# Optimization experiments

Measured on AMD Instinct MI355X. Metric: run time of the kernel, lower is better.

Reference implementation:

```python
import jax, jax.numpy as jnp
import numpy as np

B, L, D_IN, D_MODEL, H = 8, 1024, 256, 512, 8
D_HEAD = D_MODEL // H


def setup_inputs() -> dict:
    key = jax.random.key(0)
    ks = jax.random.split(key, 12)
    queries = jax.random.normal(ks[0], (B, L, D_IN), dtype=jnp.float32)
    keys_ = jax.random.normal(ks[1], (B, L, D_IN), dtype=jnp.float32)
    values = jax.random.normal(ks[2], (B, L, D_IN), dtype=jnp.float32)
    attention_mask = jnp.ones((B, L), dtype=jnp.int32)
    # binary symmetric-ish adjacency (sparse molecular graph style)
    adjacency_matrix = (jax.random.uniform(ks[3], (B, L, L)) < 0.05).astype(jnp.float32)
    distance_matrix = jax.random.uniform(ks[4], (B, L, L), dtype=jnp.float32) * 10.0
    s = 1.0 / np.sqrt(D_IN)
    W_q = jax.random.normal(ks[5], (D_MODEL, D_IN), dtype=jnp.float32) * s
    W_k = jax.random.normal(ks[6], (D_MODEL, D_IN), dtype=jnp.float32) * s
    W_v = jax.random.normal(ks[7], (D_MODEL, D_IN), dtype=jnp.float32) * s
    W_o = jax.random.normal(ks[8], (D_MODEL, D_MODEL), dtype=jnp.float32) / np.sqrt(D_MODEL)
    lambda_a = jax.random.normal(ks[9], (H,), dtype=jnp.float32) * 0.1
    lambda_d = jax.random.normal(ks[10], (H,), dtype=jnp.float32) * 0.1
    return {"queries": queries, "keys": keys_, "values": values,
            "attention_mask": attention_mask, "adjacency_matrix": adjacency_matrix,
            "distance_matrix": distance_matrix, "W_q": W_q, "W_k": W_k,
            "W_v": W_v, "W_o": W_o, "lambda_a": lambda_a, "lambda_d": lambda_d}


def _split_heads(x):
    # (b, l, d_model) -> (b, h, l, d_head)
    b, l, _ = x.shape
    return x.reshape(b, l, H, D_HEAD).transpose(0, 2, 1, 3)


def reference(queries, keys, values, attention_mask, adjacency_matrix,
              distance_matrix, W_q, W_k, W_v, W_o, lambda_a, lambda_d):
    Q = _split_heads(queries @ W_q.T)   # (b,h,l,d)
    K = _split_heads(keys @ W_k.T)
    V = _split_heads(values @ W_v.T)
    scores = jnp.einsum("bhqd,bhkd->bhqk", Q, K) / jnp.sqrt(jnp.asarray(D_HEAD, Q.dtype))
    # MSRSA: per-head learned scalars inject graph structure into the scores
    scores = (scores
              + lambda_a[None, :, None, None] * adjacency_matrix[:, None, :, :]
              + lambda_d[None, :, None, None] * distance_matrix[:, None, :, :])
    mask = attention_mask[:, None, None, :] > 0  # (b,1,1,l) key mask
    scores = jnp.where(mask, scores, jnp.asarray(-1e9, scores.dtype))
    attn_weight = jax.nn.softmax(scores, axis=-1)  # (b,h,l,l)
    out = jnp.einsum("bhqk,bhkd->bhqd", attn_weight, V)
    out = out.transpose(0, 2, 1, 3).reshape(queries.shape[0], queries.shape[1], D_MODEL)
    return out @ W_o.T
```

## Files before the change

### kernel.cpp

```cpp
#include <hip/hip_runtime.h>
#include <hip/hip_fp16.h>

#define BB 8
#define LL 1024
#define DIN 256
#define DM 512
#define HH 8
#define DH 64

typedef __attribute__((ext_vector_type(8))) short bf16x8;
typedef __attribute__((ext_vector_type(4))) float f32x4;

__device__ __forceinline__ unsigned short f2bf(float f) {
  union { float f; unsigned u; } c; c.f = f;
  unsigned u = c.u;
  return (unsigned short)((u + 0x7fffu + ((u >> 16) & 1u)) >> 16);
}

#if defined(__has_builtin)
#if __has_builtin(__builtin_amdgcn_cvt_pk_bf16_f32)
#define HAS_PK_BF16 1
#endif
#endif

#ifdef HAS_PK_BF16
typedef __bf16 bf2 __attribute__((ext_vector_type(2)));
__device__ __forceinline__ unsigned pk2(float lo, float hi) {
  union { bf2 v; unsigned u; } c;
  c.v = __builtin_amdgcn_cvt_pk_bf16_f32(lo, hi);
  return c.u;
}
#else
__device__ __forceinline__ unsigned pk2(float lo, float hi) {
  return ((unsigned)f2bf(hi) << 16) | f2bf(lo);
}
#endif

__device__ __forceinline__ unsigned pkh(float a, float d) {
  return (unsigned)__half_as_ushort(__float2half_rn(a)) |
         ((unsigned)__half_as_ushort(__float2half_rn(d)) << 16);
}

__device__ __forceinline__ void async_copy16(void* lds, const void* g) {
  __builtin_amdgcn_global_load_lds(
      (const __attribute__((address_space(1))) unsigned*)g,
      (__attribute__((address_space(3))) unsigned*)lds, 16, 0, 0);
}

__global__ __launch_bounds__(256) void prep(
    const float* __restrict__ qin, const float* __restrict__ kin,
    const float* __restrict__ vin,
    const float* __restrict__ wq, const float* __restrict__ wk,
    const float* __restrict__ wv, const float* __restrict__ wo,
    const int* __restrict__ msk,
    const float* __restrict__ adj, const float* __restrict__ dis,
    unsigned short* __restrict__ xq, unsigned short* __restrict__ xk,
    unsigned short* __restrict__ xv,
    unsigned short* __restrict__ wqb, unsigned short* __restrict__ wkb,
    unsigned short* __restrict__ wvb, unsigned short* __restrict__ wob,
    float* __restrict__ mad, unsigned* __restrict__ bp)
{
  int t = blockIdx.x * 256 + threadIdx.x;
  const int XS = 524288, WS = 32768;
  if (t < 3 * XS) {
    int seg = t >> 19, off = t & (XS - 1);
    const float* s = (seg == 0) ? qin : (seg == 1) ? kin : vin;
    unsigned short* d = (seg == 0) ? xq : (seg == 1) ? xk : xv;
    float4 f = ((const float4*)s)[off];
    uint2 o = { pk2(f.x, f.y), pk2(f.z, f.w) };
    ((uint2*)d)[off] = o;
    return;
  }
  t -= 3 * XS;
  if (t < 3 * WS) {
    int seg = t >> 15, off = t & (WS - 1);
    const float* s = (seg == 0) ? wq : (seg == 1) ? wk : wv;
    unsigned short* d = (seg == 0) ? wqb : (seg == 1) ? wkb : wvb;
    float4 f = ((const float4*)s)[off];
    uint2 o = { pk2(f.x, f.y), pk2(f.z, f.w) };
    ((uint2*)d)[off] = o;
    return;
  }
  t -= 3 * WS;
  if (t < 65536) {
    float4 f = ((const float4*)wo)[t];
    uint2 o = { pk2(f.x, f.y), pk2(f.z, f.w) };
    ((uint2*)wob)[t] = o;
    return;
  }
  t -= 65536;
  if (t < 2048) {
    int4 m = ((const int4*)msk)[t];
    float4 f = { m.x ? 0.0f : -30000.0f, m.y ? 0.0f : -30000.0f,
                 m.z ? 0.0f : -30000.0f, m.w ? 0.0f : -30000.0f };
    ((float4*)mad)[t] = f;
    return;
  }
  t -= 2048;
  float4 a4 = ((const float4*)adj)[t];
  float4 d4 = ((const float4*)dis)[t];
  uint4 o = { pkh(a4.x, d4.x), pkh(a4.y, d4.y), pkh(a4.z, d4.z), pkh(a4.w, d4.w) };
  ((uint4*)bp)[t] = o;
}

__global__ __launch_bounds__(256) void qkv_proj(
    const unsigned short* __restrict__ xq, const unsigned short* __restrict__ xk,
    const unsigned short* __restrict__ xv,
    const unsigned short* __restrict__ wqb, const unsigned short* __restrict__ wkb,
    const unsigned short* __restrict__ wvb,
    unsigned short* __restrict__ qb, unsigned short* __restrict__ kb,
    unsigned short* __restrict__ vt)
{
  const int t = blockIdx.z;
  const unsigned short* __restrict__ X = (t == 0) ? xq : (t == 1) ? xk : xv;
  const unsigned short* __restrict__ W = (t == 0) ? wqb : (t == 1) ? wkb : wvb;
  const int m0 = blockIdx.y * 128;
  const int h  = blockIdx.x;
  __shared__ __align__(16) char arena[24576];
  const int tid = threadIdx.x;
  const int wid = tid >> 6;
  const int lane = tid & 63;
  const int lo = lane & 15;
  const int quad = lane >> 4;

  f32x4 acc[2][4];
#pragma unroll
  for (int mi = 0; mi < 2; ++mi)
#pragma unroll
    for (int ni = 0; ni < 4; ++ni) acc[mi][ni] = (f32x4)0.0f;

#pragma unroll
  for (int j = 0; j < 2; ++j) {
    int id = j * 256 + tid, r = id >> 2, c = id & 3;
    async_copy16(arena + j * 4096 + wid * 1024,
                 X + (size_t)(m0 + r) * DIN + ((c ^ (r & 3)) * 8));
  }
  {
    int id = tid, r = id >> 2, c = id & 3;
    async_copy16(arena + 16384 + wid * 1024,
                 W + (size_t)(h * 64 + r) * DIN + ((c ^ (r & 3)) * 8));
  }
  __syncthreads();

  for (int it = 0; it < 8; ++it) {
    const int p = it & 1;
    if (it < 7) {
      const int kk = (it + 1) * 32, q = 1 - p;
#pragma unroll
      for (int j = 0; j < 2; ++j) {
        int id = j * 256 + tid, r = id >> 2, c = id & 3;
        async_copy16(arena + q * 8192 + j * 4096 + wid * 1024,
                     X + (size_t)(m0 + r) * DIN + kk + ((c ^ (r & 3)) * 8));
      }
      {
        int id = tid, r = id >> 2, c = id & 3;
        async_copy16(arena + 16384 + q * 4096 + wid * 1024,
                     W + (size_t)(h * 64 + r) * DIN + kk + ((c ^ (r & 3)) * 8));
      }
    }
    const unsigned short* Ab = (const unsigned short*)(arena + p * 8192);
    const unsigned short* Bb = (const unsigned short*)(arena + 16384 + p * 4096);
    bf16x8 a[2], bfr[4];
#pragma unroll
    for (int mi = 0; mi < 2; ++mi) {
      int R = wid * 32 + mi * 16 + lo;
      a[mi] = *(const bf16x8*)&Ab[R * 32 + ((quad ^ (R & 3)) * 8)];
    }
#pragma unroll
    for (int ni = 0; ni < 4; ++ni) {
      int N = ni * 16 + lo;
      bfr[ni] = *(const bf16x8*)&Bb[N * 32 + ((quad ^ (N & 3)) * 8)];
    }
#pragma unroll
    for (int mi = 0; mi < 2; ++mi)
#pragma unroll
      for (int ni = 0; ni < 4; ++ni)
        acc[mi][ni] = __builtin_amdgcn_mfma_f32_16x16x32_bf16(
            a[mi], bfr[ni], acc[mi][ni], 0, 0, 0);
    __syncthreads();
  }

  const int b = m0 >> 10;
  const int lbase0 = (m0 & 1023) + wid * 32;
  if (t < 2) {
    unsigned short* dstp = (t == 0) ? qb : kb;
#pragma unroll
    for (int mi = 0; mi < 2; ++mi)
#pragma unroll
      for (int ni = 0; ni < 4; ++ni) {
        int d = ni * 16 + lo;
#pragma unroll
        for (int r = 0; r < 4; ++r) {
          int lb = lbase0 + mi * 16 + quad * 4 + r;
          dstp[((size_t)(b * HH + h) * LL + lb) * DH + d] = f2bf(acc[mi][ni][r]);
        }
      }
  } else {
#pragma unroll
    for (int mi = 0; mi < 2; ++mi)
#pragma unroll
      for (int ni = 0; ni < 4; ++ni) {
        int d = ni * 16 + lo;
        int lb = lbase0 + mi * 16 + quad * 4;
        uint2 o = { pk2(acc[mi][ni][0], acc[mi][ni][1]),
                    pk2(acc[mi][ni][2], acc[mi][ni][3]) };
        *(uint2*)&vt[((size_t)(b * HH + h) * DH + d) * LL + lb] = o;
      }
  }
}

__global__ __launch_bounds__(256) void attn(
    const unsigned short* __restrict__ qb, const unsigned short* __restrict__ kb,
    const unsigned short* __restrict__ vt,
    const float* __restrict__ mad, const unsigned* __restrict__ bp,
    const float* __restrict__ la_, const float* __restrict__ ld_,
    unsigned short* __restrict__ ao)
{
  const int bi = blockIdx.x;
  const int b  = bi & 7;
  const int hg = (bi >> 3) & 3;
  const int q0 = (bi >> 5) * 32;
  const int tid = threadIdx.x;
  const int wid = tid >> 6;
  const int lane = tid & 63;
  const int lo = lane & 15;
  const int quad = lane >> 4;
  const int h  = hg * 2 + (wid & 1);
  const int kh = wid >> 1;
  const int bh = b * HH + h;

  __shared__ __align__(16) char arena[59392];
  unsigned short* pbufw = (unsigned short*)(arena + 49152) + wid * 1280;
  float*          mgbuf = (float*)arena;

  const float LOG2E = 1.44269504f;
  const float la2 = la_[h] * LOG2E, ld2 = ld_[h] * LOG2E;
  const float sc2 = 0.125f * LOG2E;

  const unsigned short* qp = qb + ((size_t)bh * LL + q0) * DH;
  bf16x8 qB[2][2];
#pragma unroll
  for (int nj = 0; nj < 2; ++nj)
#pragma unroll
    for (int ki = 0; ki < 2; ++ki)
      qB[nj][ki] = *(const bf16x8*)&qp[(nj * 16 + lo) * DH + ki * 32 + quad * 8];

  const unsigned short* kp = kb + (size_t)bh * LL * DH;
  const unsigned short* vp = vt + (size_t)bh * DH * LL;
  const unsigned* bpp = bp + ((size_t)b * LL + q0) * LL;
  const float* mp = mad + b * LL;

  f32x4 o[4][2];
  float rs[2] = {0.0f, 0.0f};
#pragma unroll
  for (int md = 0; md < 4; ++md)
#pragma unroll
    for (int nj = 0; nj < 2; ++nj) o[md][nj] = (f32x4)0.0f;

  const int kbeg = kh * (LL / 2);
  const int r8 = lane >> 3, p8 = lane & 7;

  {
    const unsigned short* kg = kp + (size_t)kbeg * DH;
#pragma unroll
    for (int j = 0; j < 4; ++j)
      async_copy16(arena + wid * 4096 + j * 1024,
                   kg + (j * 8 + r8) * 64 + ((p8 ^ r8) * 8));
    if ((wid & 1) == 0) {
      const int khs = wid >> 1;
      const unsigned* bg = bpp + khs * (LL / 2);
#pragma unroll
      for (int j = 0; j < 4; ++j)
        async_copy16(arena + 32768 + khs * 4096 + j * 1024,
                     bg + (size_t)(j * 8 + r8) * LL + ((p8 ^ r8) * 4));
    }
  }
  __syncthreads();

  for (int jt = 0; jt < 16; ++jt) {
    const int p = jt & 1;
    const int k0 = kbeg + jt * 32;

    if (jt < 15) {
      const int kn = k0 + 32, q = 1 - p;
      const unsigned short* kg = kp + (size_t)kn * DH;
#pragma unroll
      for (int j = 0; j < 4; ++j)
        async_copy16(arena + q * 16384 + wid * 4096 + j * 1024,
                     kg + (j * 8 + r8) * 64 + ((p8 ^ r8) * 8));
      if ((wid & 1) == 0) {
        const int khs = wid >> 1;
        const unsigned* bg = bpp + khs * (LL / 2) + (jt + 1) * 32;
#pragma unroll
        for (int j = 0; j < 4; ++j)
          async_copy16(arena + 32768 + q * 8192 + khs * 4096 + j * 1024,
                       bg + (size_t)(j * 8 + r8) * LL + ((p8 ^ r8) * 4));
      }
    }

    bf16x8 vA[4];
#pragma unroll
    for (int md = 0; md < 4; ++md)
      vA[md] = *(const bf16x8*)&vp[(md * 16 + lo) * LL + k0 + quad * 8];
    f32x4 msv[2];
#pragma unroll
    for (int mi = 0; mi < 2; ++mi)
      msv[mi] = *(const f32x4*)&mp[k0 + mi * 16 + quad * 4];

    const unsigned short* kbf = (const unsigned short*)(arena + p * 16384) + wid * 2048;
    const unsigned* bbf = (const unsigned*)(arena + 32768 + p * 8192) + kh * 1024;

    bf16x8 kA[2][2];
#pragma unroll
    for (int mi = 0; mi < 2; ++mi)
#pragma unroll
      for (int ki = 0; ki < 2; ++ki)
        kA[mi][ki] = *(const bf16x8*)&kbf[(mi * 16 + lo) * 64 +
                                          (((ki * 4 + quad) ^ (lo & 7)) * 8)];
    f32x4 s[2][2];
#pragma unroll
    for (int mi = 0; mi < 2; ++mi)
#pragma unroll
      for (int nj = 0; nj < 2; ++nj) s[mi][nj] = (f32x4)0.0f;
#pragma unroll
    for (int ki = 0; ki < 2; ++ki)
#pragma unroll
      for (int mi = 0; mi < 2; ++mi)
#pragma unroll
        for (int nj = 0; nj < 2; ++nj)
          s[mi][nj] = __builtin_amdgcn_mfma_f32_16x16x32_bf16(
              kA[mi][ki], qB[nj][ki], s[mi][nj], 0, 0, 0);

#pragma unroll
    for (int mi = 0; mi < 2; ++mi)
#pragma unroll
      for (int nj = 0; nj < 2; ++nj) {
        uint4 u = *(const uint4*)&bbf[(nj * 16 + lo) * 32 +
                                      (((mi * 4 + quad) ^ (lo & 7)) * 4)];
        float p4[4];
#pragma unroll
        for (int r = 0; r < 4; ++r) {
          union { unsigned v; __half2 hh; } c; c.v = u[r];
          float tt = fmaf(__high2float(c.hh), ld2, msv[mi][r]);
          tt = fmaf(__low2float(c.hh), la2, tt);
          p4[r] = __builtin_amdgcn_exp2f(fmaf(s[mi][nj][r], sc2, tt));
        }
        rs[nj] += (p4[0] + p4[1]) + (p4[2] + p4[3]);
        uint2 w = { pk2(p4[0], p4[1]), pk2(p4[2], p4[3]) };
        *(uint2*)&pbufw[(nj * 16 + lo) * 40 + mi * 16 + quad * 4] = w;
      }

    asm volatile("s_waitcnt lgkmcnt(0)" ::: "memory");

    bf16x8 pB[2];
#pragma unroll
    for (int nj = 0; nj < 2; ++nj)
      pB[nj] = *(const bf16x8*)&pbufw[(nj * 16 + lo) * 40 + quad * 8];

#pragma unroll
    for (int md = 0; md < 4; ++md)
#pragma unroll
      for (int nj = 0; nj < 2; ++nj)
        o[md][nj] = __builtin_amdgcn_mfma_f32_16x16x32_bf16(
            vA[md], pB[nj], o[md][nj], 0, 0, 0);

    __syncthreads();
  }

  const int hs = wid & 1;
  if (kh == 1) {
#pragma unroll
    for (int md = 0; md < 4; ++md)
#pragma unroll
      for (int nj = 0; nj < 2; ++nj)
#pragma unroll
        for (int r = 0; r < 4; ++r)
          mgbuf[hs * 2176 + ((md * 2 + nj) * 4 + r) * 64 + lane] = o[md][nj][r];
    mgbuf[hs * 2176 + 32 * 64 + lane] = rs[0];
    mgbuf[hs * 2176 + 33 * 64 + lane] = rs[1];
  }
  __syncthreads();
  if (kh == 0) {
#pragma unroll
    for (int md = 0; md < 4; ++md)
#pragma unroll
      for (int nj = 0; nj < 2; ++nj)
#pragma unroll
        for (int r = 0; r < 4; ++r)
          o[md][nj][r] += mgbuf[hs * 2176 + ((md * 2 + nj) * 4 + r) * 64 + lane];
    rs[0] += mgbuf[hs * 2176 + 32 * 64 + lane];
    rs[1] += mgbuf[hs * 2176 + 33 * 64 + lane];
    float inv[2];
#pragma unroll
    for (int nj = 0; nj < 2; ++nj) {
      rs[nj] += __shfl_xor(rs[nj], 16);
      rs[nj] += __shfl_xor(rs[nj], 32);
      inv[nj] = __builtin_amdgcn_rcpf(rs[nj]);
    }
#pragma unroll
    for (int md = 0; md < 4; ++md)
#pragma unroll
      for (int nj = 0; nj < 2; ++nj) {
        int l = q0 + nj * 16 + lo;
        uint2 st = { pk2(o[md][nj][0] * inv[nj], o[md][nj][1] * inv[nj]),
                     pk2(o[md][nj][2] * inv[nj], o[md][nj][3] * inv[nj]) };
        *(uint2*)&ao[((size_t)b * LL + l) * DM + h * DH + md * 16 + quad * 4] = st;
      }
  }
}

__global__ __launch_bounds__(256) void oproj(
    const unsigned short* __restrict__ ao, const unsigned short* __restrict__ wob,
    float* __restrict__ out)
{
  const int m0 = blockIdx.y * 128;
  const int n0 = blockIdx.x * 64;
  __shared__ __align__(16) char arena[24576];
  const int tid = threadIdx.x;
  const int wid = tid >> 6;
  const int lane = tid & 63;
  const int lo = lane & 15;
  const int quad = lane >> 4;

  f32x4 acc[2][4];
#pragma unroll
  for (int mi = 0; mi < 2; ++mi)
#pragma unroll
    for (int ni = 0; ni < 4; ++ni) acc[mi][ni] = (f32x4)0.0f;

#pragma unroll
  for (int j = 0; j < 2; ++j) {
    int id = j * 256 + tid, r = id >> 2, c = id & 3;
    async_copy16(arena + j * 4096 + wid * 1024,
                 ao + (size_t)(m0 + r) * DM + ((c ^ (r & 3)) * 8));
  }
  {
    int id = tid, r = id >> 2, c = id & 3;
    async_copy16(arena + 16384 + wid * 1024,
                 wob + (size_t)(n0 + r) * DM + ((c ^ (r & 3)) * 8));
  }
  __syncthreads();

  for (int it = 0; it < 16; ++it) {
    const int p = it & 1;
    if (it < 15) {
      const int kk = (it + 1) * 32, q = 1 - p;
#pragma unroll
      for (int j = 0; j < 2; ++j) {
        int id = j * 256 + tid, r = id >> 2, c = id & 3;
        async_copy16(arena + q * 8192 + j * 4096 + wid * 1024,
                     ao + (size_t)(m0 + r) * DM + kk + ((c ^ (r & 3)) * 8));
      }
      {
        int id = tid, r = id >> 2, c = id & 3;
        async_copy16(arena + 16384 + q * 4096 + wid * 1024,
                     wob + (size_t)(n0 + r) * DM + kk + ((c ^ (r & 3)) * 8));
      }
    }
    const unsigned short* Ab = (const unsigned short*)(arena + p * 8192);
    const unsigned short* Bb = (const unsigned short*)(arena + 16384 + p * 4096);
    bf16x8 a[2], bfr[4];
#pragma unroll
    for (int mi = 0; mi < 2; ++mi) {
      int R = wid * 32 + mi * 16 + lo;
      a[mi] = *(const bf16x8*)&Ab[R * 32 + ((quad ^ (R & 3)) * 8)];
    }
#pragma unroll
    for (int ni = 0; ni < 4; ++ni) {
      int N = ni * 16 + lo;
      bfr[ni] = *(const bf16x8*)&Bb[N * 32 + ((quad ^ (N & 3)) * 8)];
    }
#pragma unroll
    for (int mi = 0; mi < 2; ++mi)
#pragma unroll
      for (int ni = 0; ni < 4; ++ni)
        acc[mi][ni] = __builtin_amdgcn_mfma_f32_16x16x32_bf16(
            a[mi], bfr[ni], acc[mi][ni], 0, 0, 0);
    __syncthreads();
  }

#pragma unroll
  for (int mi = 0; mi < 2; ++mi)
#pragma unroll
    for (int ni = 0; ni < 4; ++ni)
#pragma unroll
      for (int r = 0; r < 4; ++r)
        out[(size_t)(m0 + wid * 32 + mi * 16 + quad * 4 + r) * DM +
            n0 + ni * 16 + lo] = acc[mi][ni][r];
}

extern "C" void kernel_launch(void* const* d_in, const int* in_sizes, int n_in,
                              void* d_out, int out_size, void* d_ws, size_t ws_size,
                              hipStream_t stream) {
  const float* qin = (const float*)d_in[0];
  const float* kin = (const float*)d_in[1];
  const float* vin = (const float*)d_in[2];
  const int*   msk = (const int*)d_in[3];
  const float* adj = (const float*)d_in[4];
  const float* dis = (const float*)d_in[5];
  const float* wq  = (const float*)d_in[6];
  const float* wk  = (const float*)d_in[7];
  const float* wv  = (const float*)d_in[8];
  const float* wo  = (const float*)d_in[9];
  const float* la  = (const float*)d_in[10];
  const float* ld  = (const float*)d_in[11];
  float* out = (float*)d_out;

  const size_t tensb = (size_t)BB * HH * LL * DH;
  const size_t xsz   = (size_t)BB * LL * DIN;
  unsigned short* qb  = (unsigned short*)d_ws;
  unsigned short* kb  = qb + tensb;
  unsigned short* vt  = kb + tensb;
  unsigned short* ao  = vt + tensb;
  unsigned short* xq  = ao;
  unsigned short* xk  = ao + xsz;
  unsigned short* xv  = ao + tensb;
  unsigned short* wqb = xv + xsz;
  unsigned short* wkb = wqb + (size_t)DM * DIN;
  unsigned short* wvb = wkb + (size_t)DM * DIN;
  unsigned short* wob = wvb + (size_t)DM * DIN;
  float*          mdd = (float*)(wob + (size_t)DM * DM);
  unsigned*       bpk = (unsigned*)(mdd + (size_t)BB * LL);

  prep<<<dim3(14984), 256, 0, stream>>>(qin, kin, vin, wq, wk, wv, wo, msk,
                                        adj, dis,
                                        xq, xk, xv, wqb, wkb, wvb, wob, mdd, bpk);
  qkv_proj<<<dim3(8, 64, 3), 256, 0, stream>>>(xq, xk, xv, wqb, wkb, wvb, qb, kb, vt);
  attn<<<dim3(1024), 256, 0, stream>>>(qb, kb, vt, mdd, bpk, la, ld, ao);
  oproj<<<dim3(8, 64), 256, 0, stream>>>(ao, wob, out);
}
```

Measured before the change: 233.9 us.

## Fuse input conversion into QKV projection and drop the separate prep pass

```diff
diff --git a/kernel.cpp b/kernel.cpp
--- a/kernel.cpp
+++ b/kernel.cpp
@@ -41,87 +41,52 @@
          ((unsigned)__half_as_ushort(__float2half_rn(d)) << 16);
 }
 
+__device__ __forceinline__ bf16x8 cvt8(f32x4 c0, f32x4 c1) {
+  union { unsigned u[4]; bf16x8 v; } r;
+  r.u[0] = pk2(c0[0], c0[1]); r.u[1] = pk2(c0[2], c0[3]);
+  r.u[2] = pk2(c1[0], c1[1]); r.u[3] = pk2(c1[2], c1[3]);
+  return r.v;
+}
+
 __device__ __forceinline__ void async_copy16(void* lds, const void* g) {
   __builtin_amdgcn_global_load_lds(
       (const __attribute__((address_space(1))) unsigned*)g,
       (__attribute__((address_space(3))) unsigned*)lds, 16, 0, 0);
 }
 
-__global__ __launch_bounds__(256) void prep(
+__global__ __launch_bounds__(256) void k1(
     const float* __restrict__ qin, const float* __restrict__ kin,
     const float* __restrict__ vin,
     const float* __restrict__ wq, const float* __restrict__ wk,
-    const float* __restrict__ wv, const float* __restrict__ wo,
-    const int* __restrict__ msk,
+    const float* __restrict__ wv,
     const float* __restrict__ adj, const float* __restrict__ dis,
-    unsigned short* __restrict__ xq, unsigned short* __restrict__ xk,
-    unsigned short* __restrict__ xv,
-    unsigned short* __restrict__ wqb, unsigned short* __restrict__ wkb,
-    unsigned short* __restrict__ wvb, unsigned short* __restrict__ wob,
-    float* __restrict__ mad, unsigned* __restrict__ bp)
+    unsigned short* __restrict__ qb, unsigned short* __restrict__ kb,
+    unsigned short* __restrict__ vt, unsigned* __restrict__ bp)
 {
-  int t = blockIdx.x * 256 + threadIdx.x;
-  const int XS = 524288, WS = 32768;
-  if (t < 3 * XS) {
-    int seg = t >> 19, off = t & (XS - 1);
-    const float* s = (seg == 0) ? qin : (seg == 1) ? kin : vin;
-    unsigned short* d = (seg == 0) ? xq : (seg == 1) ? xk : xv;
-    float4 f = ((const float4*)s)[off];
-    uint2 o = { pk2(f.x, f.y), pk2(f.z, f.w) };
-    ((uint2*)d)[off] = o;
+  __shared__ __align__(16) char arena[49152];
+  int bx = blockIdx.x;
+  if (bx < 8192) {
+    int t = bx * 256 + threadIdx.x;
+    float4 a4 = ((const float4*)adj)[t];
+    float4 d4 = ((const float4*)dis)[t];
+    uint4 o = { pkh(a4.x, d4.x), pkh(a4.y, d4.y),
+                pkh(a4.z, d4.z), pkh(a4.w, d4.w) };
+    ((uint4*)bp)[t] = o;
     return;
   }
-  t -= 3 * XS;
-  if (t < 3 * WS) {
-    int seg = t >> 15, off = t & (WS - 1);
-    const float* s = (seg == 0) ? wq : (seg == 1) ? wk : wv;
-    unsigned short* d = (seg == 0) ? wqb : (seg == 1) ? wkb : wvb;
-    float4 f = ((const float4*)s)[off];
-    uint2 o = { pk2(f.x, f.y), pk2(f.z, f.w) };
-    ((uint2*)d)[off] = o;
-    return;
-  }
-  t -= 3 * WS;
-  if (t < 65536) {
-    float4 f = ((const float4*)wo)[t];
-    uint2 o = { pk2(f.x, f.y), pk2(f.z, f.w) };
-    ((uint2*)wob)[t] = o;
-    return;
-  }
-  t -= 65536;
-  if (t < 2048) {
-    int4 m = ((const int4*)msk)[t];
-    float4 f = { m.x ? 0.0f : -30000.0f, m.y ? 0.0f : -30000.0f,
-                 m.z ? 0.0f : -30000.0f, m.w ? 0.0f : -30000.0f };
-    ((float4*)mad)[t] = f;
-    return;
-  }
-  t -= 2048;
-  float4 a4 = ((const float4*)adj)[t];
-  float4 d4 = ((const float4*)dis)[t];
-  uint4 o = { pkh(a4.x, d4.x), pkh(a4.y, d4.y), pkh(a4.z, d4.z), pkh(a4.w, d4.w) };
-  ((uint4*)bp)[t] = o;
-}
-
-__global__ __launch_bounds__(256) void qkv_proj(
-    const unsigned short* __restrict__ xq, const unsigned short* __restrict__ xk,
-    const unsigned short* __restrict__ xv,
-    const unsigned short* __restrict__ wqb, const unsigned short* __restrict__ wkb,
-    const unsigned short* __restrict__ wvb,
-    unsigned short* __restrict__ qb, unsigned short* __restrict__ kb,
-    unsigned short* __restrict__ vt)
-{
-  const int t = blockIdx.z;
-  const unsigned short* __restrict__ X = (t == 0) ? xq : (t == 1) ? xk : xv;
-  const unsigned short* __restrict__ W = (t == 0) ? wqb : (t == 1) ? wkb : wvb;
-  const int m0 = blockIdx.y * 128;
-  const int h  = blockIdx.x;
-  __shared__ __align__(16) char arena[24576];
+  bx -= 8192;
+  const int t = bx >> 9;
+  const int r_ = bx & 511;
+  const int m0 = (r_ >> 3) * 128;
+  const int h  = r_ & 7;
+  const float* __restrict__ X = (t == 0) ? qin : (t == 1) ? kin : vin;
+  const float* __restrict__ W = (t == 0) ? wq : (t == 1) ? wk : wv;
   const int tid = threadIdx.x;
   const int wid = tid >> 6;
   const int lane = tid & 63;
   const int lo = lane & 15;
   const int quad = lane >> 4;
+  const int r8 = lane >> 3, c8 = lane & 7;
 
   f32x4 acc[2][4];
 #pragma unroll
@@ -130,16 +95,13 @@
     for (int ni = 0; ni < 4; ++ni) acc[mi][ni] = (f32x4)0.0f;
 
 #pragma unroll
-  for (int j = 0; j < 2; ++j) {
-    int id = j * 256 + tid, r = id >> 2, c = id & 3;
+  for (int j = 0; j < 4; ++j)
     async_copy16(arena + j * 4096 + wid * 1024,
-                 X + (size_t)(m0 + r) * DIN + ((c ^ (r & 3)) * 8));
-  }
-  {
-    int id = tid, r = id >> 2, c = id & 3;
-    async_copy16(arena + 16384 + wid * 1024,
-                 W + (size_t)(h * 64 + r) * DIN + ((c ^ (r & 3)) * 8));
-  }
+                 X + (size_t)(m0 + j * 32 + wid * 8 + r8) * DIN + ((c8 ^ r8) * 4));
+#pragma unroll
+  for (int j = 0; j < 2; ++j)
+    async_copy16(arena + 32768 + j * 4096 + wid * 1024,
+                 W + (size_t)(h * 64 + j * 32 + wid * 8 + r8) * DIN + ((c8 ^ r8) * 4));
   __syncthreads();
 
   for (int it = 0; it < 8; ++it) {
@@ -147,29 +109,30 @@
     if (it < 7) {
       const int kk = (it + 1) * 32, q = 1 - p;
 #pragma unroll
-      for (int j = 0; j < 2; ++j) {
-        int id = j * 256 + tid, r = id >> 2, c = id & 3;
-        async_copy16(arena + q * 8192 + j * 4096 + wid * 1024,
-                     X + (size_t)(m0 + r) * DIN + kk + ((c ^ (r & 3)) * 8));
-      }
-      {
-        int id = tid, r = id >> 2, c = id & 3;
-        async_copy16(arena + 16384 + q * 4096 + wid * 1024,
-                     W + (size_t)(h * 64 + r) * DIN + kk + ((c ^ (r & 3)) * 8));
-      }
-    }
-    const unsigned short* Ab = (const unsigned short*)(arena + p * 8192);
-    const unsigned short* Bb = (const unsigned short*)(arena + 16384 + p * 4096);
+      for (int j = 0; j < 4; ++j)
+        async_copy16(arena + q * 16384 + j * 4096 + wid * 1024,
+                     X + (size_t)(m0 + j * 32 + wid * 8 + r8) * DIN + kk + ((c8 ^ r8) * 4));
+#pragma unroll
+      for (int j = 0; j < 2; ++j)
+        async_copy16(arena + 32768 + q * 8192 + j * 4096 + wid * 1024,
+                     W + (size_t)(h * 64 + j * 32 + wid * 8 + r8) * DIN + kk + ((c8 ^ r8) * 4));
+    }
+    const float* Af = (const float*)(arena + p * 16384);
+    const float* Bf = (const float*)(arena + 32768 + p * 8192);
     bf16x8 a[2], bfr[4];
 #pragma unroll
     for (int mi = 0; mi < 2; ++mi) {
       int R = wid * 32 + mi * 16 + lo;
-      a[mi] = *(const bf16x8*)&Ab[R * 32 + ((quad ^ (R & 3)) * 8)];
+      f32x4 c0 = *(const f32x4*)&Af[R * 32 + (((quad * 2) ^ (R & 7)) * 4)];
+      f32x4 c1 = *(const f32x4*)&Af[R * 32 + (((quad * 2 + 1) ^ (R & 7)) * 4)];
+      a[mi] = cvt8(c0, c1);
     }
 #pragma unroll
     for (int ni = 0; ni < 4; ++ni) {
       int N = ni * 16 + lo;
-      bfr[ni] = *(const bf16x8*)&Bb[N * 32 + ((quad ^ (N & 3)) * 8)];
+      f32x4 c0 = *(const f32x4*)&Bf[N * 32 + (((quad * 2) ^ (N & 7)) * 4)];
+      f32x4 c1 = *(const f32x4*)&Bf[N * 32 + (((quad * 2 + 1) ^ (N & 7)) * 4)];
+      bfr[ni] = cvt8(c0, c1);
     }
 #pragma unroll
     for (int mi = 0; mi < 2; ++mi)
@@ -212,7 +175,7 @@
 __global__ __launch_bounds__(256) void attn(
     const unsigned short* __restrict__ qb, const unsigned short* __restrict__ kb,
     const unsigned short* __restrict__ vt,
-    const float* __restrict__ mad, const unsigned* __restrict__ bp,
+    const int* __restrict__ msk, const unsigned* __restrict__ bp,
     const float* __restrict__ la_, const float* __restrict__ ld_,
     unsigned short* __restrict__ ao)
 {
@@ -229,8 +192,9 @@
   const int kh = wid >> 1;
   const int bh = b * HH + h;
 
-  __shared__ __align__(16) char arena[59392];
-  unsigned short* pbufw = (unsigned short*)(arena + 49152) + wid * 1280;
+  __shared__ __align__(16) char arena[41984];
+  unsigned short* kbufw = (unsigned short*)(arena) + wid * 2048;
+  unsigned short* pbufw = (unsigned short*)(arena + 32768) + wid * 1152;
   float*          mgbuf = (float*)arena;
 
   const float LOG2E = 1.44269504f;
@@ -248,7 +212,7 @@
   const unsigned short* kp = kb + (size_t)bh * LL * DH;
   const unsigned short* vp = vt + (size_t)bh * DH * LL;
   const unsigned* bpp = bp + ((size_t)b * LL + q0) * LL;
-  const float* mp = mad + b * LL;
+  const int* mp = msk + b * LL;
 
   f32x4 o[4][2];
   float rs[2] = {0.0f, 0.0f};
@@ -271,7 +235,7 @@
       const unsigned* bg = bpp + khs * (LL / 2);
 #pragma unroll
       for (int j = 0; j < 4; ++j)
-        async_copy16(arena + 32768 + khs * 4096 + j * 1024,
+        async_copy16(arena + 16384 + khs * 4096 + j * 1024,
                      bg + (size_t)(j * 8 + r8) * LL + ((p8 ^ r8) * 4));
     }
   }
@@ -281,42 +245,22 @@
     const int p = jt & 1;
     const int k0 = kbeg + jt * 32;
 
-    if (jt < 15) {
-      const int kn = k0 + 32, q = 1 - p;
-      const unsigned short* kg = kp + (size_t)kn * DH;
-#pragma unroll
-      for (int j = 0; j < 4; ++j)
-        async_copy16(arena + q * 16384 + wid * 4096 + j * 1024,
-                     kg + (j * 8 + r8) * 64 + ((p8 ^ r8) * 8));
-      if ((wid & 1) == 0) {
-        const int khs = wid >> 1;
-        const unsigned* bg = bpp + khs * (LL / 2) + (jt + 1) * 32;
-#pragma unroll
-        for (int j = 0; j < 4; ++j)
-          async_copy16(arena + 32768 + q * 8192 + khs * 4096 + j * 1024,
-                       bg + (size_t)(j * 8 + r8) * LL + ((p8 ^ r8) * 4));
-      }
-    }
-
     bf16x8 vA[4];
 #pragma unroll
     for (int md = 0; md < 4; ++md)
       vA[md] = *(const bf16x8*)&vp[(md * 16 + lo) * LL + k0 + quad * 8];
-    f32x4 msv[2];
-#pragma unroll
-    for (int mi = 0; mi < 2; ++mi)
-      msv[mi] = *(const f32x4*)&mp[k0 + mi * 16 + quad * 4];
-
-    const unsigned short* kbf = (const unsigned short*)(arena + p * 16384) + wid * 2048;
-    const unsigned* bbf = (const unsigned*)(arena + 32768 + p * 8192) + kh * 1024;
+    int4 mv[2];
+#pragma unroll
+    for (int mi = 0; mi < 2; ++mi)
+      mv[mi] = *(const int4*)&mp[k0 + mi * 16 + quad * 4];
 
     bf16x8 kA[2][2];
 #pragma unroll
     for (int mi = 0; mi < 2; ++mi)
 #pragma unroll
       for (int ki = 0; ki < 2; ++ki)
-        kA[mi][ki] = *(const bf16x8*)&kbf[(mi * 16 + lo) * 64 +
-                                          (((ki * 4 + quad) ^ (lo & 7)) * 8)];
+        kA[mi][ki] = *(const bf16x8*)&kbufw[(mi * 16 + lo) * 64 +
+                                            (((ki * 4 + quad) ^ (lo & 7)) * 8)];
     f32x4 s[2][2];
 #pragma unroll
     for (int mi = 0; mi < 2; ++mi)
@@ -331,31 +275,57 @@
           s[mi][nj] = __builtin_amdgcn_mfma_f32_16x16x32_bf16(
               kA[mi][ki], qB[nj][ki], s[mi][nj], 0, 0, 0);
 
+    asm volatile("s_waitcnt lgkmcnt(0)\n\ts_barrier" ::: "memory");
+
+    if (jt < 15) {
+      const unsigned short* kg = kp + (size_t)(k0 + 32) * DH;
+#pragma unroll
+      for (int j = 0; j < 4; ++j)
+        async_copy16(arena + wid * 4096 + j * 1024,
+                     kg + (j * 8 + r8) * 64 + ((p8 ^ r8) * 8));
+    }
+
+    const unsigned* bbp = (const unsigned*)(arena + 16384 + p * 8192) + kh * 1024;
+    float msvf[2][4];
+#pragma unroll
+    for (int mi = 0; mi < 2; ++mi)
+#pragma unroll
+      for (int r = 0; r < 4; ++r)
+        msvf[mi][r] = ((&mv[mi].x)[r] != 0) ? 0.0f : -30000.0f;
 #pragma unroll
     for (int mi = 0; mi < 2; ++mi)
 #pragma unroll
       for (int nj = 0; nj < 2; ++nj) {
-        uint4 u = *(const uint4*)&bbf[(nj * 16 + lo) * 32 +
+        uint4 u = *(const uint4*)&bbp[(nj * 16 + lo) * 32 +
                                       (((mi * 4 + quad) ^ (lo & 7)) * 4)];
         float p4[4];
 #pragma unroll
         for (int r = 0; r < 4; ++r) {
           union { unsigned v; __half2 hh; } c; c.v = u[r];
-          float tt = fmaf(__high2float(c.hh), ld2, msv[mi][r]);
+          float tt = fmaf(__high2float(c.hh), ld2, msvf[mi][r]);
           tt = fmaf(__low2float(c.hh), la2, tt);
           p4[r] = __builtin_amdgcn_exp2f(fmaf(s[mi][nj][r], sc2, tt));
         }
         rs[nj] += (p4[0] + p4[1]) + (p4[2] + p4[3]);
         uint2 w = { pk2(p4[0], p4[1]), pk2(p4[2], p4[3]) };
-        *(uint2*)&pbufw[(nj * 16 + lo) * 40 + mi * 16 + quad * 4] = w;
+        *(uint2*)&pbufw[(nj * 16 + lo) * 36 + mi * 16 + quad * 4] = w;
       }
 
+    if (jt < 15 && (wid & 1) == 0) {
+      const int khs = wid >> 1;
+      const unsigned* bg = bpp + khs * (LL / 2) + (jt + 1) * 32;
+#pragma unroll
+      for (int j = 0; j < 4; ++j)
+        async_copy16(arena + 16384 + (1 - p) * 8192 + khs * 4096 + j * 1024,
+                     bg + (size_t)(j * 8 + r8) * LL + ((p8 ^ r8) * 4));
+    }
+
     asm volatile("s_waitcnt lgkmcnt(0)" ::: "memory");
 
     bf16x8 pB[2];
 #pragma unroll
     for (int nj = 0; nj < 2; ++nj)
-      pB[nj] = *(const bf16x8*)&pbufw[(nj * 16 + lo) * 40 + quad * 8];
+      pB[nj] = *(const bf16x8*)&pbufw[(nj * 16 + lo) * 36 + quad * 8];
 
 #pragma unroll
     for (int md = 0; md < 4; ++md)
@@ -410,17 +380,19 @@
 }
 
 __global__ __launch_bounds__(256) void oproj(
-    const unsigned short* __restrict__ ao, const unsigned short* __restrict__ wob,
+    const unsigned short* __restrict__ ao, const float* __restrict__ wo,
     float* __restrict__ out)
 {
   const int m0 = blockIdx.y * 128;
   const int n0 = blockIdx.x * 64;
-  __shared__ __align__(16) char arena[24576];
+  __shared__ __align__(16) char arena[32768];
   const int tid = threadIdx.x;
   const int wid = tid >> 6;
   const int lane = tid & 63;
   const int lo = lane & 15;
   const int quad = lane >> 4;
+  const int r8 = lane >> 3, c8 = lane & 7;
+  const int r4 = lane >> 2, c4 = lane & 3;
 
   f32x4 acc[2][4];
 #pragma unroll
@@ -429,16 +401,13 @@
     for (int ni = 0; ni < 4; ++ni) acc[mi][ni] = (f32x4)0.0f;
 
 #pragma unroll
-  for (int j = 0; j < 2; ++j) {
-    int id = j * 256 + tid, r = id >> 2, c = id & 3;
+  for (int j = 0; j < 2; ++j)
     async_copy16(arena + j * 4096 + wid * 1024,
-                 ao + (size_t)(m0 + r) * DM + ((c ^ (r & 3)) * 8));
-  }
-  {
-    int id = tid, r = id >> 2, c = id & 3;
-    async_copy16(arena + 16384 + wid * 1024,
-                 wob + (size_t)(n0 + r) * DM + ((c ^ (r & 3)) * 8));
-  }
+                 ao + (size_t)(m0 + j * 64 + wid * 16 + r4) * DM + ((c4 ^ (r4 & 3)) * 8));
+#pragma unroll
+  for (int j = 0; j < 2; ++j)
+    async_copy16(arena + 16384 + j * 4096 + wid * 1024,
+                 wo + (size_t)(n0 + j * 32 + wid * 8 + r8) * DM + ((c8 ^ r8) * 4));
   __syncthreads();
 
   for (int it = 0; it < 16; ++it) {
@@ -446,19 +415,16 @@
     if (it < 15) {
       const int kk = (it + 1) * 32, q = 1 - p;
 #pragma unroll
-      for (int j = 0; j < 2; ++j) {
-        int id = j * 256 + tid, r = id >> 2, c = id & 3;
+      for (int j = 0; j < 2; ++j)
         async_copy16(arena + q * 8192 + j * 4096 + wid * 1024,
-                     ao + (size_t)(m0 + r) * DM + kk + ((c ^ (r & 3)) * 8));
-      }
-      {
-        int id = tid, r = id >> 2, c = id & 3;
-        async_copy16(arena + 16384 + q * 4096 + wid * 1024,
-                     wob + (size_t)(n0 + r) * DM + kk + ((c ^ (r & 3)) * 8));
-      }
+                     ao + (size_t)(m0 + j * 64 + wid * 16 + r4) * DM + kk + ((c4 ^ (r4 & 3)) * 8));
+#pragma unroll
+      for (int j = 0; j < 2; ++j)
+        async_copy16(arena + 16384 + q * 8192 + j * 4096 + wid * 1024,
+                     wo + (size_t)(n0 + j * 32 + wid * 8 + r8) * DM + kk + ((c8 ^ r8) * 4));
     }
     const unsigned short* Ab = (const unsigned short*)(arena + p * 8192);
-    const unsigned short* Bb = (const unsigned short*)(arena + 16384 + p * 4096);
+    const float* Bf = (const float*)(arena + 16384 + p * 8192);
     bf16x8 a[2], bfr[4];
 #pragma unroll
     for (int mi = 0; mi < 2; ++mi) {
@@ -468,7 +434,9 @@
 #pragma unroll
     for (int ni = 0; ni < 4; ++ni) {
       int N = ni * 16 + lo;
-      bfr[ni] = *(const bf16x8*)&Bb[N * 32 + ((quad ^ (N & 3)) * 8)];
+      f32x4 c0 = *(const f32x4*)&Bf[N * 32 + (((quad * 2) ^ (N & 7)) * 4)];
+      f32x4 c1 = *(const f32x4*)&Bf[N * 32 + (((quad * 2 + 1) ^ (N & 7)) * 4)];
+      bfr[ni] = cvt8(c0, c1);
     }
 #pragma unroll
     for (int mi = 0; mi < 2; ++mi)
@@ -507,25 +475,14 @@
   float* out = (float*)d_out;
 
   const size_t tensb = (size_t)BB * HH * LL * DH;
-  const size_t xsz   = (size_t)BB * LL * DIN;
   unsigned short* qb  = (unsigned short*)d_ws;
   unsigned short* kb  = qb + tensb;
   unsigned short* vt  = kb + tensb;
   unsigned short* ao  = vt + tensb;
-  unsigned short* xq  = ao;
-  unsigned short* xk  = ao + xsz;
-  unsigned short* xv  = ao + tensb;
-  unsigned short* wqb = xv + xsz;
-  unsigned short* wkb = wqb + (size_t)DM * DIN;
-  unsigned short* wvb = wkb + (size_t)DM * DIN;
-  unsigned short* wob = wvb + (size_t)DM * DIN;
-  float*          mdd = (float*)(wob + (size_t)DM * DM);
-  unsigned*       bpk = (unsigned*)(mdd + (size_t)BB * LL);
-
-  prep<<<dim3(14984), 256, 0, stream>>>(qin, kin, vin, wq, wk, wv, wo, msk,
-                                        adj, dis,
-                                        xq, xk, xv, wqb, wkb, wvb, wob, mdd, bpk);
-  qkv_proj<<<dim3(8, 64, 3), 256, 0, stream>>>(xq, xk, xv, wqb, wkb, wvb, qb, kb, vt);
-  attn<<<dim3(1024), 256, 0, stream>>>(qb, kb, vt, mdd, bpk, la, ld, ao);
-  oproj<<<dim3(8, 64), 256, 0, stream>>>(ao, wob, out);
-}
+  unsigned*       bpk = (unsigned*)(ao + tensb);
+
+  k1<<<dim3(9728), 256, 0, stream>>>(qin, kin, vin, wq, wk, wv, adj, dis,
+                                     qb, kb, vt, bpk);
+  attn<<<dim3(1024), 256, 0, stream>>>(qb, kb, vt, msk, bpk, la, ld, ao);
+  oproj<<<dim3(8, 64), 256, 0, stream>>>(ao, wo, out);
+}
```

Measured after the change: 257.0 us. +9.9%, slower.
